# Kernel tuning notes

Hardware: AMD Instinct MI355X
Metric: run time of the kernel (lower is better)

The kernel has to match this reference:

```python
import jax, jax.numpy as jnp
import numpy as np


def setup_inputs() -> dict:
    key = jax.random.key(0)
    ks = jax.random.split(key, 3)
    B, D, U, E, T = 16384, 512, 128, 16, 4
    x = jax.random.normal(ks[0], (B, D), dtype=jnp.float32)
    expert_kernels = jax.random.normal(ks[1], (D, U, E), dtype=jnp.float32) * (1.0 / np.sqrt(D))
    expert_bias = jnp.zeros((U, E), dtype=jnp.float32)
    gate_kernels = jax.random.normal(ks[2], (T, D, E), dtype=jnp.float32) * (1.0 / np.sqrt(D))
    gate_bias = jnp.zeros((T, E), dtype=jnp.float32)
    return {"x": x, "expert_kernels": expert_kernels, "expert_bias": expert_bias,
            "gate_kernels": gate_kernels, "gate_bias": gate_bias}


def reference(x, expert_kernels, expert_bias, gate_kernels, gate_bias):
    # Experts: [B, U, E] = relu(x @ W_e + b_e)
    expert_out = jnp.einsum('bd,due->bue', x, expert_kernels) + expert_bias[None]
    expert_out = jax.nn.relu(expert_out)
    # Gates: per-task softmax over experts -> [T, B, E]
    gate_logits = jnp.einsum('bd,tde->tbe', x, gate_kernels) + gate_bias[:, None, :]
    gates = jax.nn.softmax(gate_logits, axis=-1)
    # Gated combination: [T, B, U]
    outs = jnp.einsum('bue,tbe->tbu', expert_out, gates)
    return tuple(outs[t] for t in range(outs.shape[0]))
```

## Files before the change

### kernel.cpp

```cpp
#include <hip/hip_runtime.h>


#define Bsz 16384
#define Dd  512
#define Uu  128
#define Ee  16
#define Tt  4
#define Nn  2048

typedef short bf16x8 __attribute__((ext_vector_type(8)));
typedef float f32x4 __attribute__((ext_vector_type(4)));
typedef unsigned short u16x8 __attribute__((ext_vector_type(8)));

static __device__ __forceinline__ unsigned short f2bf(float f) {
    unsigned int u = __builtin_bit_cast(unsigned int, f);
    u += 0x7fffu + ((u >> 16) & 1u);
    return (unsigned short)(u >> 16);
}
static __device__ __forceinline__ float bf2f(unsigned short s) {
    return __builtin_bit_cast(float, (unsigned int)s << 16);
}

#define GLOAD16(g, l) __builtin_amdgcn_global_load_lds( \
    (const __attribute__((address_space(1))) void*)(g), \
    (__attribute__((address_space(3))) void*)(l), 16, 0, 0)

#define GLD 72
__global__ __launch_bounds__(256) void prep_kernel(
        const float* __restrict__ x, const float* __restrict__ gk,
        const float* __restrict__ gb, const float* __restrict__ ek,
        float* __restrict__ gates, unsigned short* __restrict__ xb,
        unsigned short* __restrict__ ekT) {
    __shared__ __align__(16) unsigned short pm[4 * 64 * GLD];
    const int tid = threadIdx.x;
    if (blockIdx.x >= 256) {
        unsigned short* ts = pm;
        const int b2 = blockIdx.x - 256;
        const int n0 = (b2 & 31) * 64, d0 = (b2 >> 5) * 64;
        #pragma unroll
        for (int i = 0; i < 4; ++i) {
            int flat = i * 256 + tid;
            int dl = flat >> 4, ng = (flat & 15) * 4;
            const float4 v = *(const float4*)(ek + (size_t)(d0 + dl) * Nn + n0 + ng);
            ts[(ng + 0) * 65 + dl] = f2bf(v.x);
            ts[(ng + 1) * 65 + dl] = f2bf(v.y);
            ts[(ng + 2) * 65 + dl] = f2bf(v.z);
            ts[(ng + 3) * 65 + dl] = f2bf(v.w);
        }
        __syncthreads();
        #pragma unroll
        for (int i = 0; i < 4; ++i) {
            int flat = i * 256 + tid;
            int nl = flat >> 4, dg = (flat & 15) * 4;
            ushort4 w = make_ushort4(ts[nl * 65 + dg], ts[nl * 65 + dg + 1],
                                     ts[nl * 65 + dg + 2], ts[nl * 65 + dg + 3]);
            *(ushort4*)(ekT + (size_t)(n0 + nl) * Dd + d0 + dg) = w;
        }
        return;
    }
    unsigned short* sAh = pm;
    unsigned short* sAl = pm + 64 * GLD;
    unsigned short* sBh = pm + 2 * 64 * GLD;
    unsigned short* sBl = pm + 3 * 64 * GLD;
    const int w = tid >> 6, lane = tid & 63;
    const int llo = lane & 15, lhi = lane >> 4;
    const int b0 = blockIdx.x * 64;
    f32x4 acc[4] = {};

    for (int c = 0; c < 8; ++c) {
        const int d0 = c * 64;
        __syncthreads();
        #pragma unroll
        for (int p = 0; p < 4; ++p) {
            const int flat = p * 256 + tid;
            const int row = flat >> 4, c4 = (flat & 15) * 4;
            const float4 v = *(const float4*)(x + (size_t)(b0 + row) * Dd + d0 + c4);
            unsigned short h0 = f2bf(v.x), h1 = f2bf(v.y), h2 = f2bf(v.z), h3 = f2bf(v.w);
            const ushort4 hv = make_ushort4(h0, h1, h2, h3);
            *(ushort4*)(sAh + row * GLD + c4) = hv;
            *(ushort4*)(sAl + row * GLD + c4) = make_ushort4(
                f2bf(v.x - bf2f(h0)), f2bf(v.y - bf2f(h1)),
                f2bf(v.z - bf2f(h2)), f2bf(v.w - bf2f(h3)));
            *(ushort4*)(xb + (size_t)(b0 + row) * Dd + d0 + c4) = hv;
        }
        #pragma unroll
        for (int p = 0; p < 4; ++p) {
            const int f = p * 256 + tid;
            const int t_ = f >> 8, dl = (f >> 2) & 63, e4 = f & 3;
            const float4 v = *(const float4*)(gk + (size_t)t_ * (Dd * Ee)
                                              + (size_t)(d0 + dl) * Ee + e4 * 4);
            const int nb = t_ * 16 + e4 * 4;
            unsigned short h0 = f2bf(v.x), h1 = f2bf(v.y), h2 = f2bf(v.z), h3 = f2bf(v.w);
            sBh[(nb + 0) * GLD + dl] = h0;
            sBh[(nb + 1) * GLD + dl] = h1;
            sBh[(nb + 2) * GLD + dl] = h2;
            sBh[(nb + 3) * GLD + dl] = h3;
            sBl[(nb + 0) * GLD + dl] = f2bf(v.x - bf2f(h0));
            sBl[(nb + 1) * GLD + dl] = f2bf(v.y - bf2f(h1));
            sBl[(nb + 2) * GLD + dl] = f2bf(v.z - bf2f(h2));
            sBl[(nb + 3) * GLD + dl] = f2bf(v.w - bf2f(h3));
        }
        __syncthreads();
        #pragma unroll
        for (int ks = 0; ks < 64; ks += 32) {
            const bf16x8 ah = *(const bf16x8*)(sAh + (w * 16 + llo) * GLD + ks + lhi * 8);
            const bf16x8 al = *(const bf16x8*)(sAl + (w * 16 + llo) * GLD + ks + lhi * 8);
            #pragma unroll
            for (int ni = 0; ni < 4; ++ni) {
                const bf16x8 bh = *(const bf16x8*)(sBh + (ni * 16 + llo) * GLD + ks + lhi * 8);
                const bf16x8 bl = *(const bf16x8*)(sBl + (ni * 16 + llo) * GLD + ks + lhi * 8);
                acc[ni] = __builtin_amdgcn_mfma_f32_16x16x32_bf16(ah, bh, acc[ni], 0, 0, 0);
                acc[ni] = __builtin_amdgcn_mfma_f32_16x16x32_bf16(al, bh, acc[ni], 0, 0, 0);
                acc[ni] = __builtin_amdgcn_mfma_f32_16x16x32_bf16(ah, bl, acc[ni], 0, 0, 0);
            }
        }
    }
    #pragma unroll
    for (int ni = 0; ni < 4; ++ni) {
        const float bias = gb[ni * 16 + llo];
        #pragma unroll
        for (int j = 0; j < 4; ++j) {
            float lg = acc[ni][j] + bias;
            float m = lg;
            m = fmaxf(m, __shfl_xor(m, 1));
            m = fmaxf(m, __shfl_xor(m, 2));
            m = fmaxf(m, __shfl_xor(m, 4));
            m = fmaxf(m, __shfl_xor(m, 8));
            float p = __expf(lg - m);
            float s = p;
            s += __shfl_xor(s, 1);
            s += __shfl_xor(s, 2);
            s += __shfl_xor(s, 4);
            s += __shfl_xor(s, 8);
            const int row = b0 + w * 16 + lhi * 4 + j;
            gates[(size_t)row * 64 + ni * 16 + llo] = p / s;
        }
    }
}

#define BM 128
#define BN 256
#define BK 32

#define ST_A(buf, kt_) {                                                        \
    const int c_ = wave * 64 + lane;                                            \
    const int r_ = c_ >> 2;                                                     \
    const int l_ = (c_ & 3) ^ ((r_ >> 2) & 3);                                  \
    GLOAD16(xb + (size_t)(b0 + r_) * Dd + (kt_) * BK + l_ * 8,                  \
            smem + (buf) * 24576 + c_ * 16); }
#define ST_B(buf, kt_) { _Pragma("unroll")                                      \
    for (int i_ = 0; i_ < 2; ++i_) {                                            \
        const int c_ = i_ * 512 + wave * 64 + lane;                             \
        const int r_ = c_ >> 2;                                                 \
        const int l_ = (c_ & 3) ^ ((r_ >> 2) & 3);                              \
        GLOAD16(ekT + (size_t)(n0 + r_) * Dd + (kt_) * BK + l_ * 8,             \
                smem + (buf) * 24576 + 8192 + c_ * 16); } }
#define STAGE(buf, kt_) { ST_A(buf, kt_) ST_B(buf, kt_) }

__global__ __launch_bounds__(512) void moe_kernel(
        const unsigned short* __restrict__ xb,
        const unsigned short* __restrict__ ekT,
        const float* __restrict__ eb, const float* __restrict__ gates,
        float* __restrict__ out) {
    __shared__ __align__(64) char smem[73728];
    const int tid = threadIdx.x;
    const int wave = tid >> 6, lane = tid & 63;
    const int llo = lane & 15, lhi = lane >> 4;
    const int g = (blockIdx.x & 7) * 128 + (blockIdx.x >> 3);
    const int b0 = (g >> 3) * BM;
    const int n0 = (g & 7) * BN;
    const int mr = (wave >> 2) * 64, nc = (wave & 3) * 64;
    f32x4 acc[4][4] = {};

    STAGE(0, 0);
    STAGE(1, 1);
    for (int kt = 0; kt < Dd / BK; ++kt) {
        const char* aB = smem + (kt % 3) * 24576;
        const char* bB = aB + 8192;
        if (kt < 15) asm volatile("s_waitcnt vmcnt(3)\ns_barrier" ::: "memory");
        else         asm volatile("s_waitcnt vmcnt(0)\ns_barrier" ::: "memory");
        if (kt < 14) STAGE((kt + 2) % 3, kt + 2);
        {
            const int ph = (lhi ^ (llo >> 2)) << 4;
            bf16x8 aF[4], bF[4];
            #pragma unroll
            for (int mi = 0; mi < 4; ++mi)
                aF[mi] = *(const bf16x8*)(aB + (mr + mi * 16 + llo) * 64 + ph);
            #pragma unroll
            for (int ni = 0; ni < 4; ++ni)
                bF[ni] = *(const bf16x8*)(bB + (nc + ni * 16 + llo) * 64 + ph);
            __builtin_amdgcn_s_setprio(1);
            #pragma unroll
            for (int mi = 0; mi < 4; ++mi)
                #pragma unroll
                for (int ni = 0; ni < 4; ++ni)
                    acc[mi][ni] = __builtin_amdgcn_mfma_f32_16x16x32_bf16(
                        aF[mi], bF[ni], acc[mi][ni], 0, 0, 0);
            __builtin_amdgcn_s_setprio(0);
        }
    }
    __syncthreads();

    unsigned short* eo = (unsigned short*)smem;
    #pragma unroll
    for (int ni = 0; ni < 4; ++ni) {
        const int col = nc + ni * 16 + llo;
        const float ebv = eb[n0 + col];
        #pragma unroll
        for (int mi = 0; mi < 4; ++mi) {
            #pragma unroll
            for (int j = 0; j < 4; ++j) {
                int row = mr + mi * 16 + lhi * 4 + j;
                eo[row * 264 + col] = f2bf(fmaxf(acc[mi][ni][j] + ebv, 0.f));
            }
        }
    }
    __syncthreads();
    #pragma unroll
    for (int i = 0; i < 4; ++i) {
        int f = i * 512 + tid;
        int m = f >> 4, ul = f & 15;
        const unsigned short* er = eo + m * 264 + ul * 16;
        const float* gr = gates + (size_t)(b0 + m) * 64;
        float o0 = 0.f, o1 = 0.f, o2 = 0.f, o3 = 0.f;
        #pragma unroll
        for (int e = 0; e < 16; ++e) {
            float v = bf2f(er[e]);
            o0 = fmaf(v, gr[e], o0);
            o1 = fmaf(v, gr[16 + e], o1);
            o2 = fmaf(v, gr[32 + e], o2);
            o3 = fmaf(v, gr[48 + e], o3);
        }
        size_t base = (size_t)(b0 + m) * Uu + (n0 >> 4) + ul;
        out[base] = o0;
        out[(size_t)Bsz * Uu + base] = o1;
        out[2 * (size_t)Bsz * Uu + base] = o2;
        out[3 * (size_t)Bsz * Uu + base] = o3;
    }
}

extern "C" void kernel_launch(void* const* d_in, const int* in_sizes, int n_in,
                              void* d_out, int out_size, void* d_ws, size_t ws_size,
                              hipStream_t stream) {
    const float* x  = (const float*)d_in[0];
    const float* ek = (const float*)d_in[1];
    const float* eb = (const float*)d_in[2];
    const float* gk = (const float*)d_in[3];
    const float* gb = (const float*)d_in[4];
    float* out = (float*)d_out;

    char* wsb = (char*)d_ws;
    float* gates       = (float*)wsb;
    unsigned short* xb  = (unsigned short*)(wsb + (4u << 20));
    unsigned short* ekT = (unsigned short*)(wsb + (20u << 20));

    prep_kernel<<<512, 256, 0, stream>>>(x, gk, gb, ek, gates, xb, ekT);
    moe_kernel<<<(Bsz / BM) * (Nn / BN), 512, 0, stream>>>(xb, ekT, eb, gates, out);
}
```

Before: 84.81 us.

## Load MFMA operands directly from global memory instead of LDS pipeline

```diff
diff --git a/kernel.cpp b/kernel.cpp
--- a/kernel.cpp
+++ b/kernel.cpp
@@ -20,10 +20,6 @@
 static __device__ __forceinline__ float bf2f(unsigned short s) {
     return __builtin_bit_cast(float, (unsigned int)s << 16);
 }
-
-#define GLOAD16(g, l) __builtin_amdgcn_global_load_lds( \
-    (const __attribute__((address_space(1))) void*)(g), \
-    (__attribute__((address_space(3))) void*)(l), 16, 0, 0)
 
 #define GLD 72
 __global__ __launch_bounds__(256) void prep_kernel(
@@ -142,27 +138,12 @@
 #define BN 256
 #define BK 32
 
-#define ST_A(buf, kt_) {                                                        \
-    const int c_ = wave * 64 + lane;                                            \
-    const int r_ = c_ >> 2;                                                     \
-    const int l_ = (c_ & 3) ^ ((r_ >> 2) & 3);                                  \
-    GLOAD16(xb + (size_t)(b0 + r_) * Dd + (kt_) * BK + l_ * 8,                  \
-            smem + (buf) * 24576 + c_ * 16); }
-#define ST_B(buf, kt_) { _Pragma("unroll")                                      \
-    for (int i_ = 0; i_ < 2; ++i_) {                                            \
-        const int c_ = i_ * 512 + wave * 64 + lane;                             \
-        const int r_ = c_ >> 2;                                                 \
-        const int l_ = (c_ & 3) ^ ((r_ >> 2) & 3);                              \
-        GLOAD16(ekT + (size_t)(n0 + r_) * Dd + (kt_) * BK + l_ * 8,             \
-                smem + (buf) * 24576 + 8192 + c_ * 16); } }
-#define STAGE(buf, kt_) { ST_A(buf, kt_) ST_B(buf, kt_) }
-
 __global__ __launch_bounds__(512) void moe_kernel(
         const unsigned short* __restrict__ xb,
         const unsigned short* __restrict__ ekT,
         const float* __restrict__ eb, const float* __restrict__ gates,
         float* __restrict__ out) {
-    __shared__ __align__(64) char smem[73728];
+    __shared__ __align__(16) unsigned short eoh[64 * 264];
     const int tid = threadIdx.x;
     const int wave = tid >> 6, lane = tid & 63;
     const int llo = lane & 15, lhi = lane >> 4;
@@ -170,72 +151,77 @@
     const int b0 = (g >> 3) * BM;
     const int n0 = (g & 7) * BN;
     const int mr = (wave >> 2) * 64, nc = (wave & 3) * 64;
+    const int wr = wave >> 2;
     f32x4 acc[4][4] = {};
 
-    STAGE(0, 0);
-    STAGE(1, 1);
+    const unsigned short* aP[4];
+    const unsigned short* bP[4];
+    #pragma unroll
+    for (int mi = 0; mi < 4; ++mi)
+        aP[mi] = xb + (size_t)(b0 + mr + mi * 16 + llo) * Dd + lhi * 8;
+    #pragma unroll
+    for (int ni = 0; ni < 4; ++ni)
+        bP[ni] = ekT + (size_t)(n0 + nc + ni * 16 + llo) * Dd + lhi * 8;
+
+    #pragma unroll 4
     for (int kt = 0; kt < Dd / BK; ++kt) {
-        const char* aB = smem + (kt % 3) * 24576;
-        const char* bB = aB + 8192;
-        if (kt < 15) asm volatile("s_waitcnt vmcnt(3)\ns_barrier" ::: "memory");
-        else         asm volatile("s_waitcnt vmcnt(0)\ns_barrier" ::: "memory");
-        if (kt < 14) STAGE((kt + 2) % 3, kt + 2);
-        {
-            const int ph = (lhi ^ (llo >> 2)) << 4;
-            bf16x8 aF[4], bF[4];
-            #pragma unroll
-            for (int mi = 0; mi < 4; ++mi)
-                aF[mi] = *(const bf16x8*)(aB + (mr + mi * 16 + llo) * 64 + ph);
+        bf16x8 aF[4], bF[4];
+        #pragma unroll
+        for (int mi = 0; mi < 4; ++mi)
+            aF[mi] = *(const bf16x8*)(aP[mi] + kt * BK);
+        #pragma unroll
+        for (int ni = 0; ni < 4; ++ni)
+            bF[ni] = *(const bf16x8*)(bP[ni] + kt * BK);
+        __builtin_amdgcn_s_setprio(1);
+        #pragma unroll
+        for (int mi = 0; mi < 4; ++mi)
             #pragma unroll
             for (int ni = 0; ni < 4; ++ni)
-                bF[ni] = *(const bf16x8*)(bB + (nc + ni * 16 + llo) * 64 + ph);
-            __builtin_amdgcn_s_setprio(1);
-            #pragma unroll
-            for (int mi = 0; mi < 4; ++mi)
+                acc[mi][ni] = __builtin_amdgcn_mfma_f32_16x16x32_bf16(
+                    aF[mi], bF[ni], acc[mi][ni], 0, 0, 0);
+        __builtin_amdgcn_s_setprio(0);
+    }
+
+    #pragma unroll
+    for (int pass = 0; pass < 2; ++pass) {
+        __syncthreads();
+        if (wr == pass) {
+            #pragma unroll
+            for (int ni = 0; ni < 4; ++ni) {
+                const int col = nc + ni * 16 + llo;
+                const float ebv = eb[n0 + col];
                 #pragma unroll
-                for (int ni = 0; ni < 4; ++ni)
-                    acc[mi][ni] = __builtin_amdgcn_mfma_f32_16x16x32_bf16(
-                        aF[mi], bF[ni], acc[mi][ni], 0, 0, 0);
-            __builtin_amdgcn_s_setprio(0);
-        }
-    }
-    __syncthreads();
-
-    unsigned short* eo = (unsigned short*)smem;
-    #pragma unroll
-    for (int ni = 0; ni < 4; ++ni) {
-        const int col = nc + ni * 16 + llo;
-        const float ebv = eb[n0 + col];
-        #pragma unroll
-        for (int mi = 0; mi < 4; ++mi) {
-            #pragma unroll
-            for (int j = 0; j < 4; ++j) {
-                int row = mr + mi * 16 + lhi * 4 + j;
-                eo[row * 264 + col] = f2bf(fmaxf(acc[mi][ni][j] + ebv, 0.f));
+                for (int mi = 0; mi < 4; ++mi)
+                    #pragma unroll
+                    for (int j = 0; j < 4; ++j) {
+                        const int rl = mi * 16 + lhi * 4 + j;
+                        eoh[rl * 264 + col] = f2bf(fmaxf(acc[mi][ni][j] + ebv, 0.f));
+                    }
             }
         }
-    }
-    __syncthreads();
-    #pragma unroll
-    for (int i = 0; i < 4; ++i) {
-        int f = i * 512 + tid;
-        int m = f >> 4, ul = f & 15;
-        const unsigned short* er = eo + m * 264 + ul * 16;
-        const float* gr = gates + (size_t)(b0 + m) * 64;
-        float o0 = 0.f, o1 = 0.f, o2 = 0.f, o3 = 0.f;
-        #pragma unroll
-        for (int e = 0; e < 16; ++e) {
-            float v = bf2f(er[e]);
-            o0 = fmaf(v, gr[e], o0);
-            o1 = fmaf(v, gr[16 + e], o1);
-            o2 = fmaf(v, gr[32 + e], o2);
-            o3 = fmaf(v, gr[48 + e], o3);
-        }
-        size_t base = (size_t)(b0 + m) * Uu + (n0 >> 4) + ul;
-        out[base] = o0;
-        out[(size_t)Bsz * Uu + base] = o1;
-        out[2 * (size_t)Bsz * Uu + base] = o2;
-        out[3 * (size_t)Bsz * Uu + base] = o3;
+        __syncthreads();
+        #pragma unroll
+        for (int i = 0; i < 2; ++i) {
+            const int f = i * 512 + tid;
+            const int ml = f >> 4, ul = f & 15;
+            const unsigned short* er = eoh + ml * 264 + ul * 16;
+            const int brow = b0 + pass * 64 + ml;
+            const float* gr = gates + (size_t)brow * 64;
+            float o0 = 0.f, o1 = 0.f, o2 = 0.f, o3 = 0.f;
+            #pragma unroll
+            for (int e = 0; e < 16; ++e) {
+                const float v = bf2f(er[e]);
+                o0 = fmaf(v, gr[e], o0);
+                o1 = fmaf(v, gr[16 + e], o1);
+                o2 = fmaf(v, gr[32 + e], o2);
+                o3 = fmaf(v, gr[48 + e], o3);
+            }
+            const size_t base = (size_t)brow * Uu + (n0 >> 4) + ul;
+            out[base] = o0;
+            out[(size_t)Bsz * Uu + base] = o1;
+            out[2 * (size_t)Bsz * Uu + base] = o2;
+            out[3 * (size_t)Bsz * Uu + base] = o3;
+        }
     }
 }
 
```

Result: slower. 176.1 us (+107.6%).
